# Performance work log

Hardware: AMD Instinct MI355X
Metric: run time of the kernel (lower is better)

Reference implementation:

```python
import jax, jax.numpy as jnp
import numpy as np

B, H, S, D = 2, 16, 2048, 64

def setup_inputs() -> dict:
    key = jax.random.key(0)
    kq, kk, kv, km, ks = jax.random.split(key, 5)
    return {
        "query_input": jax.random.normal(kq, (B, H, S, D), dtype=jnp.float32),
        "key_input": jax.random.normal(kk, (B, H, S, D), dtype=jnp.float32),
        "value_input": jax.random.normal(kv, (B, H, S, D), dtype=jnp.float32),
        "query_mask": jnp.ones((B, 1, S, 1), dtype=jnp.float32),
        "key_mask": jax.random.uniform(km, (B, 1, 1, S), dtype=jnp.float32),
        "scale_factor": jax.random.normal(ks, (B, 1, 1, 1), dtype=jnp.float32),
        "dropout": 0,
    }

def reference(query_input, key_input, value_input, query_mask, key_mask, scale_factor, dropout):
    # qk = q @ k^T  -> [B, H, S, S]
    qk = jnp.einsum("bhqd,bhkd->bhqk", query_input, key_input)
    scaled_qk = qk * scale_factor                      # elementwise per-batch scale
    softmax_qk = jax.nn.softmax(scaled_qk, axis=-1)
    masked = softmax_qk * key_mask                     # post-softmax multiplicative mask
    # dropout with p=0 is the identity (deterministic baseline)
    output = jnp.einsum("bhqk,bhkd->bhqd", masked, value_input)
    return output
```

## Files before the change

kernel.cpp:

```cpp
#include <hip/hip_runtime.h>
#include <hip/hip_bf16.h>
#include <stdint.h>

#define BB 2
#define HH 16
#define SS 2048
#define DD 64
constexpr int BH = BB * HH;
constexpr int NT = SS / 64;
constexpr int QB = 16;

typedef _Float16 f16_t;
typedef f16_t f16x8 __attribute__((ext_vector_type(8)));
typedef float f32x4 __attribute__((ext_vector_type(4)));

__device__ __forceinline__ uint32_t pkf16(float a, float b) {
    return __builtin_bit_cast(uint32_t, __builtin_amdgcn_cvt_pkrtz(a, b));
}

__global__ __launch_bounds__(512)
void fattn6(const float* __restrict__ Qg, const float* __restrict__ Kg,
            const float* __restrict__ Vg, const float* __restrict__ Mg,
            const float* __restrict__ Sg, float* __restrict__ Og)
{
    __shared__ __align__(16) f16_t Kh_lds[64][72];
    __shared__ __align__(16) f16_t Vt_lds[64][72];
    __shared__ __align__(16) f16_t Pt_lds[8][16][72];
    __shared__ float msk_lds[SS];

    const int bh   = blockIdx.x % BH;
    const int qt   = blockIdx.x / BH;
    const int b    = bh / HH;
    const int tid  = threadIdx.x;
    const int wave = tid >> 6;
    const int lane = tid & 63;
    const int l16  = lane & 15;
    const int quad = lane >> 4;

    const float sc = Sg[b] * 1.44269504088896340736f;
    const size_t base = (size_t)bh * SS * DD;
    const int q0 = qt * 128 + wave * 16;

    for (int i = tid; i < SS; i += 512) msk_lds[i] = Mg[(size_t)b * SS + i];

    f16x8 qf[2];
    {
        const float* qp = Qg + base + (size_t)(q0 + l16) * DD + quad * 8;
#pragma unroll
        for (int kc = 0; kc < 2; ++kc) {
            float4 a  = *(const float4*)(qp + kc * 32);
            float4 b4 = *(const float4*)(qp + kc * 32 + 4);
            f16x8 f;
            f[0] = (f16_t)(a.x * sc);  f[1] = (f16_t)(a.y * sc);
            f[2] = (f16_t)(a.z * sc);  f[3] = (f16_t)(a.w * sc);
            f[4] = (f16_t)(b4.x * sc); f[5] = (f16_t)(b4.y * sc);
            f[6] = (f16_t)(b4.z * sc); f[7] = (f16_t)(b4.w * sc);
            qf[kc] = f;
        }
    }

    f32x4 Ot[4];
#pragma unroll
    for (int mt = 0; mt < 4; ++mt) Ot[mt] = f32x4{0.f, 0.f, 0.f, 0.f};
    float m_run = -1e30f, l_run = 0.0f;

    const int krow = tid >> 3;
    const int kc8  = (tid & 7) * 8;
    const int vd   = tid & 63;
    const int vk0  = (tid >> 6) * 8;

    for (int kt = 0; kt < NT; ++kt) {
        __syncthreads();

        {
            const float* kp = Kg + base + (size_t)(kt * 64 + krow) * DD + kc8;
            float4 a0 = *(const float4*)(kp);
            float4 a1 = *(const float4*)(kp + 4);
            uint4 w = make_uint4(pkf16(a0.x, a0.y), pkf16(a0.z, a0.w),
                                 pkf16(a1.x, a1.y), pkf16(a1.z, a1.w));
            *(uint4*)&Kh_lds[krow][kc8] = w;
        }
        {
            const float* vp = Vg + base + (size_t)(kt * 64 + vk0) * DD + vd;
            const float* mp = &msk_lds[kt * 64 + vk0];
            float v0 = vp[0 * DD] * mp[0], v1 = vp[1 * DD] * mp[1];
            float v2 = vp[2 * DD] * mp[2], v3 = vp[3 * DD] * mp[3];
            float v4 = vp[4 * DD] * mp[4], v5 = vp[5 * DD] * mp[5];
            float v6 = vp[6 * DD] * mp[6], v7 = vp[7 * DD] * mp[7];
            uint4 w = make_uint4(pkf16(v0, v1), pkf16(v2, v3),
                                 pkf16(v4, v5), pkf16(v6, v7));
            *(uint4*)&Vt_lds[vd][vk0] = w;
        }
        __syncthreads();

        f32x4 Sfr[4];
#pragma unroll
        for (int mt = 0; mt < 4; ++mt) {
            f32x4 acc = f32x4{0.f, 0.f, 0.f, 0.f};
#pragma unroll
            for (int kc = 0; kc < 2; ++kc) {
                f16x8 kh = *(const f16x8*)&Kh_lds[mt * 16 + l16][kc * 32 + quad * 8];
                acc = __builtin_amdgcn_mfma_f32_16x16x32_f16(kh, qf[kc], acc, 0, 0, 0);
            }
            Sfr[mt] = acc;
        }

        float mx = Sfr[0][0];
#pragma unroll
        for (int mt = 0; mt < 4; ++mt)
#pragma unroll
            for (int r = 0; r < 4; ++r) mx = fmaxf(mx, Sfr[mt][r]);
        mx = fmaxf(mx, __shfl_xor(mx, 16));
        mx = fmaxf(mx, __shfl_xor(mx, 32));

        if (__any(mx > m_run)) {
            const float mnew  = fmaxf(m_run, mx);
            const float alpha = exp2f(m_run - mnew);
            m_run = mnew;
            l_run *= alpha;
#pragma unroll
            for (int mt = 0; mt < 4; ++mt) Ot[mt] *= alpha;
        }

        float ps[4][4];
        float rs = 0.0f;
#pragma unroll
        for (int mt = 0; mt < 4; ++mt)
#pragma unroll
            for (int r = 0; r < 4; ++r) {
                ps[mt][r] = exp2f(Sfr[mt][r] - m_run);
                rs += ps[mt][r];
            }
        rs += __shfl_xor(rs, 16);
        rs += __shfl_xor(rs, 32);
        l_run += rs;

#pragma unroll
        for (int mt = 0; mt < 4; ++mt) {
            uint2 w = make_uint2(pkf16(ps[mt][0], ps[mt][1]),
                                 pkf16(ps[mt][2], ps[mt][3]));
            *(uint2*)&Pt_lds[wave][l16][mt * 16 + quad * 4] = w;
        }

#pragma unroll
        for (int kc = 0; kc < 2; ++kc) {
            f16x8 pf = *(const f16x8*)&Pt_lds[wave][l16][kc * 32 + quad * 8];
#pragma unroll
            for (int mt = 0; mt < 4; ++mt) {
                f16x8 vf = *(const f16x8*)&Vt_lds[mt * 16 + l16][kc * 32 + quad * 8];
                Ot[mt] = __builtin_amdgcn_mfma_f32_16x16x32_f16(vf, pf, Ot[mt], 0, 0, 0);
            }
        }
    }

    const float inv = 1.0f / l_run;
    float* op = Og + base + (size_t)(q0 + l16) * DD + quad * 4;
#pragma unroll
    for (int mt = 0; mt < 4; ++mt) {
#pragma unroll
        for (int r = 0; r < 4; ++r)
            op[mt * 16 + r] = Ot[mt][r] * inv;
    }
}

extern "C" void kernel_launch(void* const* d_in, const int* in_sizes, int n_in,
                              void* d_out, int out_size, void* d_ws, size_t ws_size,
                              hipStream_t stream) {
    const float* Qg = (const float*)d_in[0];
    const float* Kg = (const float*)d_in[1];
    const float* Vg = (const float*)d_in[2];
    const float* Mg = (const float*)d_in[4];
    const float* Sg = (const float*)d_in[5];
    float* Og = (float*)d_out;

    fattn6<<<dim3(BH * QB), dim3(512), 0, stream>>>(Qg, Kg, Vg, Mg, Sg, Og);
}
```

Before: 171.0 us.

## Prepack K/V to swizzled fp16 tiles and double-buffer via direct global-to-LDS loads

Adds a prepack kernel that converts K and mask-scaled, transposed V into fp16 tiles in workspace memory, using an XOR swizzle to avoid LDS bank conflicts. The attention kernel then streams these tiles into double-buffered LDS with global_load_lds, prefetching the next tile while the current one is computed. This removes the per-block redundant fp32-to-fp16 conversion and V transposition that all 16 query-tile blocks repeated. In exchange it adds an extra kernel launch and a pass over K/V in workspace. It falls back to the old kernel if the workspace is too small.

```diff
diff --git a/kernel.cpp b/kernel.cpp
--- a/kernel.cpp
+++ b/kernel.cpp
@@ -16,6 +16,196 @@
 
 __device__ __forceinline__ uint32_t pkf16(float a, float b) {
     return __builtin_bit_cast(uint32_t, __builtin_amdgcn_cvt_pkrtz(a, b));
+}
+
+__global__ __launch_bounds__(256)
+void prepack(const float* __restrict__ Kg, const float* __restrict__ Vg,
+             const float* __restrict__ Mg, f16_t* __restrict__ Kp,
+             f16_t* __restrict__ Vp)
+{
+    __shared__ float Vs[64][65];
+    const int bh = blockIdx.x % BH;
+    const int kt = blockIdx.x / BH;
+    const int b  = bh / HH;
+    const int t  = threadIdx.x;
+    const size_t gbase = (size_t)bh * SS * DD + (size_t)kt * 64 * DD;
+    const size_t tbase = ((size_t)bh * NT + kt) * 4096;
+
+    for (int c = t; c < 512; c += 256) {
+        const int row = c >> 3, j = c & 7;
+        const float* kp = Kg + gbase + (size_t)row * DD + j * 8;
+        float4 a = *(const float4*)kp;
+        float4 d = *(const float4*)(kp + 4);
+        uint4 w = make_uint4(pkf16(a.x, a.y), pkf16(a.z, a.w),
+                             pkf16(d.x, d.y), pkf16(d.z, d.w));
+        *(uint4*)&Kp[tbase + (size_t)row * 64 + ((j ^ (row & 7)) * 8)] = w;
+    }
+
+    for (int c = t; c < 1024; c += 256) {
+        const int key = c >> 4, dc = (c & 15) * 4;
+        float4 v = *(const float4*)(Vg + gbase + (size_t)key * DD + dc);
+        const float m = Mg[(size_t)b * SS + kt * 64 + key];
+        Vs[key][dc + 0] = v.x * m;
+        Vs[key][dc + 1] = v.y * m;
+        Vs[key][dc + 2] = v.z * m;
+        Vs[key][dc + 3] = v.w * m;
+    }
+    __syncthreads();
+
+    for (int c = t; c < 512; c += 256) {
+        const int dr = c >> 3, j = c & 7;
+        float v0 = Vs[j * 8 + 0][dr], v1 = Vs[j * 8 + 1][dr];
+        float v2 = Vs[j * 8 + 2][dr], v3 = Vs[j * 8 + 3][dr];
+        float v4 = Vs[j * 8 + 4][dr], v5 = Vs[j * 8 + 5][dr];
+        float v6 = Vs[j * 8 + 6][dr], v7 = Vs[j * 8 + 7][dr];
+        uint4 w = make_uint4(pkf16(v0, v1), pkf16(v2, v3),
+                             pkf16(v4, v5), pkf16(v6, v7));
+        *(uint4*)&Vp[tbase + (size_t)dr * 64 + ((j ^ (dr & 7)) * 8)] = w;
+    }
+}
+
+__global__ __launch_bounds__(512)
+void fattn7(const float* __restrict__ Qg, const f16_t* __restrict__ Kp,
+            const f16_t* __restrict__ Vp, const float* __restrict__ Sg,
+            float* __restrict__ Og)
+{
+    __shared__ __align__(16) f16_t Kt[2][4096];
+    __shared__ __align__(16) f16_t Vt[2][4096];
+    __shared__ __align__(16) f16_t Pt[8][16][72];
+
+    const int bh   = blockIdx.x % BH;
+    const int qt   = blockIdx.x / BH;
+    const int b    = bh / HH;
+    const int tid  = threadIdx.x;
+    const int wave = tid >> 6;
+    const int lane = tid & 63;
+    const int l16  = lane & 15;
+    const int quad = lane >> 4;
+
+    const float sc = Sg[b] * 1.44269504088896340736f;
+    const size_t base = (size_t)bh * SS * DD;
+    const size_t tb0  = (size_t)bh * NT * 4096;
+    const int q0 = qt * 128 + wave * 16;
+
+    auto stage = [&](int kt, int buf) {
+        const f16_t* ks = Kp + tb0 + (size_t)kt * 4096 + tid * 8;
+        const f16_t* vs = Vp + tb0 + (size_t)kt * 4096 + tid * 8;
+        __builtin_amdgcn_global_load_lds(
+            (const __attribute__((address_space(1))) void*)ks,
+            (__attribute__((address_space(3))) void*)&Kt[buf][wave * 512],
+            16, 0, 0);
+        __builtin_amdgcn_global_load_lds(
+            (const __attribute__((address_space(1))) void*)vs,
+            (__attribute__((address_space(3))) void*)&Vt[buf][wave * 512],
+            16, 0, 0);
+    };
+
+    stage(0, 0);
+
+    f16x8 qf[2];
+    {
+        const float* qp = Qg + base + (size_t)(q0 + l16) * DD + quad * 8;
+#pragma unroll
+        for (int kc = 0; kc < 2; ++kc) {
+            float4 a  = *(const float4*)(qp + kc * 32);
+            float4 b4 = *(const float4*)(qp + kc * 32 + 4);
+            f16x8 f;
+            f[0] = (f16_t)(a.x * sc);  f[1] = (f16_t)(a.y * sc);
+            f[2] = (f16_t)(a.z * sc);  f[3] = (f16_t)(a.w * sc);
+            f[4] = (f16_t)(b4.x * sc); f[5] = (f16_t)(b4.y * sc);
+            f[6] = (f16_t)(b4.z * sc); f[7] = (f16_t)(b4.w * sc);
+            qf[kc] = f;
+        }
+    }
+
+    f32x4 Ot[4];
+#pragma unroll
+    for (int mt = 0; mt < 4; ++mt) Ot[mt] = f32x4{0.f, 0.f, 0.f, 0.f};
+    float m_run = -1e30f, l_run = 0.0f;
+
+    const int swz = (l16 & 7) << 3;
+
+    for (int kt = 0; kt < NT; ++kt) {
+        const int cur = kt & 1;
+        if (kt + 1 < NT) {
+            stage(kt + 1, cur ^ 1);
+            asm volatile("s_waitcnt vmcnt(2)" ::: "memory");
+        } else {
+            asm volatile("s_waitcnt vmcnt(0)" ::: "memory");
+        }
+        __builtin_amdgcn_s_barrier();
+
+        f32x4 Sfr[4];
+#pragma unroll
+        for (int mt = 0; mt < 4; ++mt) {
+            f32x4 acc = f32x4{0.f, 0.f, 0.f, 0.f};
+#pragma unroll
+            for (int kc = 0; kc < 2; ++kc) {
+                const int off = (mt * 16 + l16) * 64 + ((kc * 32 + quad * 8) ^ swz);
+                f16x8 kh = *(const f16x8*)&Kt[cur][off];
+                acc = __builtin_amdgcn_mfma_f32_16x16x32_f16(kh, qf[kc], acc, 0, 0, 0);
+            }
+            Sfr[mt] = acc;
+        }
+
+        float m0 = fmaxf(fmaxf(Sfr[0][0], Sfr[0][1]), fmaxf(Sfr[0][2], Sfr[0][3]));
+        float m1 = fmaxf(fmaxf(Sfr[1][0], Sfr[1][1]), fmaxf(Sfr[1][2], Sfr[1][3]));
+        float m2 = fmaxf(fmaxf(Sfr[2][0], Sfr[2][1]), fmaxf(Sfr[2][2], Sfr[2][3]));
+        float m3 = fmaxf(fmaxf(Sfr[3][0], Sfr[3][1]), fmaxf(Sfr[3][2], Sfr[3][3]));
+        float mx = fmaxf(fmaxf(m0, m1), fmaxf(m2, m3));
+        mx = fmaxf(mx, __shfl_xor(mx, 16));
+        mx = fmaxf(mx, __shfl_xor(mx, 32));
+
+        if (__any(mx > m_run)) {
+            const float mnew  = fmaxf(m_run, mx);
+            const float alpha = exp2f(m_run - mnew);
+            m_run = mnew;
+            l_run *= alpha;
+#pragma unroll
+            for (int mt = 0; mt < 4; ++mt) Ot[mt] *= alpha;
+        }
+
+        float ps[4][4];
+        float rs = 0.0f;
+#pragma unroll
+        for (int mt = 0; mt < 4; ++mt)
+#pragma unroll
+            for (int r = 0; r < 4; ++r) {
+                ps[mt][r] = exp2f(Sfr[mt][r] - m_run);
+                rs += ps[mt][r];
+            }
+        rs += __shfl_xor(rs, 16);
+        rs += __shfl_xor(rs, 32);
+        l_run += rs;
+
+#pragma unroll
+        for (int mt = 0; mt < 4; ++mt) {
+            uint2 w = make_uint2(pkf16(ps[mt][0], ps[mt][1]),
+                                 pkf16(ps[mt][2], ps[mt][3]));
+            *(uint2*)&Pt[wave][l16][mt * 16 + quad * 4] = w;
+        }
+
+#pragma unroll
+        for (int kc = 0; kc < 2; ++kc) {
+            f16x8 pf = *(const f16x8*)&Pt[wave][l16][kc * 32 + quad * 8];
+#pragma unroll
+            for (int mt = 0; mt < 4; ++mt) {
+                const int off = (mt * 16 + l16) * 64 + ((kc * 32 + quad * 8) ^ swz);
+                f16x8 vf = *(const f16x8*)&Vt[cur][off];
+                Ot[mt] = __builtin_amdgcn_mfma_f32_16x16x32_f16(vf, pf, Ot[mt], 0, 0, 0);
+            }
+        }
+        __builtin_amdgcn_s_barrier();
+    }
+
+    const float inv = 1.0f / l_run;
+    float* op = Og + base + (size_t)(q0 + l16) * DD + quad * 4;
+#pragma unroll
+    for (int mt = 0; mt < 4; ++mt) {
+#pragma unroll
+        for (int r = 0; r < 4; ++r)
+            op[mt * 16 + r] = Ot[mt][r] * inv;
+    }
 }
 
 __global__ __launch_bounds__(512)
@@ -71,7 +261,6 @@
 
     for (int kt = 0; kt < NT; ++kt) {
         __syncthreads();
-
         {
             const float* kp = Kg + base + (size_t)(kt * 64 + krow) * DD + kc8;
             float4 a0 = *(const float4*)(kp);
@@ -173,5 +362,15 @@
     const float* Sg = (const float*)d_in[5];
     float* Og = (float*)d_out;
 
-    fattn6<<<dim3(BH * QB), dim3(512), 0, stream>>>(Qg, Kg, Vg, Mg, Sg, Og);
-}
+    const size_t kv_elems = (size_t)BH * SS * DD;
+    const size_t need = 2 * kv_elems * sizeof(f16_t);
+
+    if (d_ws != nullptr && ws_size >= need) {
+        f16_t* Kp = (f16_t*)d_ws;
+        f16_t* Vp = Kp + kv_elems;
+        prepack<<<dim3(BH * NT), dim3(256), 0, stream>>>(Kg, Vg, Mg, Kp, Vp);
+        fattn7<<<dim3(BH * QB), dim3(512), 0, stream>>>(Qg, Kp, Vp, Sg, Og);
+    } else {
+        fattn6<<<dim3(BH * QB), dim3(512), 0, stream>>>(Qg, Kg, Vg, Mg, Sg, Og);
+    }
+}
```

After: 170.7 us. About the same (-0.1%).
